# Kernel tuning notes

Hardware: AMD Instinct MI355X
Metric: run time of the kernel (lower is better)

## Reference

```python
import jax, jax.numpy as jnp
import numpy as np

B, S, D, H = 2, 2048, 1024, 16
DH = D // H  # 64, matches Attention's hardcoded d_k=64 scale


def setup_inputs() -> dict:
    key = jax.random.key(0)
    kq, kk, kv, kw, kb = jax.random.split(key, 5)
    return {
        "q": jax.random.normal(kq, (B, S, D), dtype=jnp.float32),
        "k": jax.random.normal(kk, (B, S, D), dtype=jnp.float32),
        "v": jax.random.normal(kv, (B, S, D), dtype=jnp.float32),
        "w_o_w": jax.random.normal(kw, (D, D), dtype=jnp.float32) * 0.02,
        "w_o_b": jax.random.normal(kb, (D,), dtype=jnp.float32) * 0.02,
    }


def _to_heads(x):
    # [B,S,D] -> [B,H,S,DH]
    b, s, d = x.shape
    return x.reshape(b, s, H, DH).transpose(0, 2, 1, 3)


def reference(q, k, v, w_o_w, w_o_b):
    # pre-activation (F.relu) on raw q,k,v
    qh = _to_heads(jax.nn.relu(q))
    kh = _to_heads(jax.nn.relu(k))
    vh = _to_heads(jax.nn.relu(v))
    scale = 1.0 / jnp.sqrt(jnp.asarray(DH, dtype=q.dtype))
    # naive attention: full [B,H,S,S] score matrix, softmax over keys
    scores = jnp.einsum("bhsd,bhtd->bhst", qh, kh) * scale
    probs = jax.nn.softmax(scores, axis=-1)
    attn = jnp.einsum("bhst,bhtd->bhsd", probs, vh)
    # merge heads: [B,H,S,DH] -> [B,S,D]
    out = attn.transpose(0, 2, 1, 3).reshape(B, S, D)
    # output projection (nn.Linear applies x @ W.T + b) then post-activation
    out = out @ w_o_w.T + w_o_b
    return jax.nn.relu(out)
```

## Files before the change

### kernel.cpp

```cpp
#include <hip/hip_runtime.h>
#include <hip/hip_bf16.h>

#define Bc 2
#define Hc 16
#define Sc 2048
#define Dc 1024

typedef __attribute__((ext_vector_type(8))) short s16x8;
typedef __attribute__((ext_vector_type(4))) float f32x4;
typedef __attribute__((ext_vector_type(16))) float f32x16;

#define AS1 __attribute__((address_space(1)))
#define AS3 __attribute__((address_space(3)))

static __device__ __forceinline__ float fexp2(float x) {
#if __has_builtin(__builtin_amdgcn_exp2f)
    return __builtin_amdgcn_exp2f(x);
#else
    float r; asm("v_exp_f32 %0, %1" : "=v"(r) : "v"(x)); return r;
#endif
}

static __device__ __forceinline__ unsigned cvtpk(float lo, float hi) {
    unsigned r; asm("v_cvt_pk_bf16_f32 %0, %1, %2" : "=v"(r) : "v"(lo), "v"(hi));
    return r;
}

static __device__ __forceinline__ void plswap(unsigned &x, unsigned &y) {
#if __has_builtin(__builtin_amdgcn_permlane32_swap)
    typedef __attribute__((ext_vector_type(2))) unsigned int u32x2;
    u32x2 t = __builtin_amdgcn_permlane32_swap(x, y, false, false);
    x = t.x; y = t.y;
#else
    asm volatile("v_permlane32_swap_b32 %0, %1" : "+v"(x), "+v"(y));
#endif
}

static __device__ __forceinline__ unsigned short f2bf(float f) {
    union { float f; unsigned u; } x; x.f = f;
    unsigned r = x.u + 0x7fffu + ((x.u >> 16) & 1u);
    return (unsigned short)(r >> 16);
}

__global__ __launch_bounds__(256) void relu_cvt_heads(const float* __restrict__ src,
                                                      unsigned short* __restrict__ dst,
                                                      float scale) {
    long i = ((long)blockIdx.x * blockDim.x + threadIdx.x) * 4;
    if (i >= (long)Bc * Sc * Dc) return;
    int dh = (int)(i & 63);
    int h  = (int)((i >> 6) & (Hc - 1));
    int s  = (int)((i >> 10) & (Sc - 1));
    int b  = (int)(i >> 21);
    float4 v = *reinterpret_cast<const float4*>(src + i);
    long o = (((long)b * Hc + h) * Sc + s) * 64 + dh;
    ushort4 w;
    w.x = f2bf(fmaxf(v.x, 0.f) * scale);
    w.y = f2bf(fmaxf(v.y, 0.f) * scale);
    w.z = f2bf(fmaxf(v.z, 0.f) * scale);
    w.w = f2bf(fmaxf(v.w, 0.f) * scale);
    *reinterpret_cast<ushort4*>(dst + o) = w;
}

__global__ __launch_bounds__(256) void relu_cvt_vT(const float* __restrict__ v,
                                                   unsigned short* __restrict__ vt) {
    __shared__ unsigned short lds[64][66];
    const int tid = threadIdx.x;
    const int st = blockIdx.x & (Sc / 64 - 1);
    const int bh = blockIdx.x >> 5;
    const int b = bh >> 4, h = bh & 15;
#pragma unroll
    for (int i = 0; i < 4; ++i) {
        int srow = (tid >> 4) + i * 16;
        int scol = (tid & 15) * 4;
        float4 x = *(const float4*)(v + ((long)b * Sc + st * 64 + srow) * Dc + h * 64 + scol);
        lds[srow][scol + 0] = f2bf(fmaxf(x.x, 0.f));
        lds[srow][scol + 1] = f2bf(fmaxf(x.y, 0.f));
        lds[srow][scol + 2] = f2bf(fmaxf(x.z, 0.f));
        lds[srow][scol + 3] = f2bf(fmaxf(x.w, 0.f));
    }
    __syncthreads();
#pragma unroll
    for (int i = 0; i < 2; ++i) {
        int dh = (tid >> 3) + i * 32;
        int sc = (tid & 7) * 8;
        union { unsigned short u[8]; s16x8 v8; } o;
#pragma unroll
        for (int j = 0; j < 8; ++j) o.u[j] = lds[sc + j][dh];
        *(s16x8*)(vt + ((long)bh * 64 + dh) * Sc + st * 64 + sc) = o.v8;
    }
}

__global__ __launch_bounds__(256) void cvt_w(const float* __restrict__ src,
                                             unsigned short* __restrict__ dst) {
    long i = ((long)blockIdx.x * blockDim.x + threadIdx.x) * 4;
    if (i >= (long)Dc * Dc) return;
    float4 v = *reinterpret_cast<const float4*>(src + i);
    ushort4 w;
    w.x = f2bf(v.x); w.y = f2bf(v.y); w.z = f2bf(v.z); w.w = f2bf(v.w);
    *reinterpret_cast<ushort4*>(dst + i) = w;
}

__global__ __launch_bounds__(256, 2) void attn_lds(const unsigned short* __restrict__ qh,
                                                   const unsigned short* __restrict__ kh,
                                                   const unsigned short* __restrict__ vt,
                                                   unsigned short* __restrict__ xout) {
    __shared__ unsigned short Klds[2][64 * 64];
    __shared__ unsigned short Vlds[2][64 * 64];

    const int tid = threadIdx.x;
    const int l = tid & 63, w = tid >> 6;
    const int r32 = l & 31, hl = l >> 5;
    const int job = (blockIdx.x & 7) * 64 + (blockIdx.x >> 3);
    const int qb = job & 15;
    const int bh = job >> 4;

    const unsigned short* Qp = qh + ((long)bh * Sc + qb * 128 + w * 32) * 64;
    const unsigned short* Kp = kh + (long)bh * Sc * 64;
    const unsigned short* Vp = vt + (long)bh * 64 * Sc;

    s16x8 qbf[4];
#pragma unroll
    for (int ds = 0; ds < 4; ++ds)
        qbf[ds] = *(const s16x8*)(Qp + r32 * 64 + ds * 16 + hl * 8);

    f32x16 acc0 = {0,0,0,0,0,0,0,0,0,0,0,0,0,0,0,0};
    f32x16 acc1 = {0,0,0,0,0,0,0,0,0,0,0,0,0,0,0,0};
    float denom = 0.f;

    auto stage = [&](int buf, int kv0) {
#pragma unroll
        for (int j = 0; j < 2; ++j) {
            const int cbase = w * 64 + j * 256;
            const int chunk = cbase + l;
            const int row = chunk >> 3, cc = chunk & 7;
            const int scc = cc ^ (row & 7);
            const unsigned short* ksrc = Kp + (long)(kv0 + row) * 64 + scc * 8;
            const unsigned short* vsrc = Vp + (long)row * Sc + kv0 + scc * 8;
            __builtin_amdgcn_global_load_lds((const AS1 unsigned int*)(const void*)ksrc,
                                             (AS3 unsigned int*)(void*)&Klds[buf][cbase * 8],
                                             16, 0, 0);
            __builtin_amdgcn_global_load_lds((const AS1 unsigned int*)(const void*)vsrc,
                                             (AS3 unsigned int*)(void*)&Vlds[buf][cbase * 8],
                                             16, 0, 0);
        }
    };

    auto compute = [&](int buf) {
        const unsigned short* KB = &Klds[buf][0];
        const unsigned short* VB = &Vlds[buf][0];
        unsigned Bw[4][4];
#pragma unroll
        for (int kt = 0; kt < 2; ++kt) {
            f32x16 st = {0,0,0,0,0,0,0,0,0,0,0,0,0,0,0,0};
#pragma unroll
            for (int ds = 0; ds < 4; ++ds) {
                const int row = kt * 32 + r32;
                const int cc = ((ds * 2 + hl) ^ (row & 7));
                s16x8 ka = *(const s16x8*)(KB + row * 64 + cc * 8);
                st = __builtin_amdgcn_mfma_f32_32x32x16_bf16(ka, qbf[ds], st, 0, 0, 0);
            }
            float p[16];
#pragma unroll
            for (int i = 0; i < 16; ++i) p[i] = fexp2(st[i]);
            denom += (((p[0] + p[1]) + (p[2] + p[3])) + ((p[4] + p[5]) + (p[6] + p[7])))
                   + (((p[8] + p[9]) + (p[10] + p[11])) + ((p[12] + p[13]) + (p[14] + p[15])));
            unsigned a0 = cvtpk(p[0], p[1]),   b0 = cvtpk(p[2], p[3]);
            unsigned c0 = cvtpk(p[4], p[5]),   d0 = cvtpk(p[6], p[7]);
            unsigned a1 = cvtpk(p[8], p[9]),   b1 = cvtpk(p[10], p[11]);
            unsigned c1 = cvtpk(p[12], p[13]), d1 = cvtpk(p[14], p[15]);
            plswap(a0, c0); plswap(b0, d0);
            plswap(a1, c1); plswap(b1, d1);
            Bw[kt * 2 + 0][0] = a0; Bw[kt * 2 + 0][1] = b0;
            Bw[kt * 2 + 0][2] = c0; Bw[kt * 2 + 0][3] = d0;
            Bw[kt * 2 + 1][0] = a1; Bw[kt * 2 + 1][1] = b1;
            Bw[kt * 2 + 1][2] = c1; Bw[kt * 2 + 1][3] = d1;
        }
#pragma unroll
        for (int dt = 0; dt < 2; ++dt) {
#pragma unroll
            for (int s = 0; s < 4; ++s) {
                const int row = dt * 32 + r32;
                const int cc = ((s * 2 + hl) ^ (row & 7));
                s16x8 va = *(const s16x8*)(VB + row * 64 + cc * 8);
                union { unsigned u[4]; s16x8 v8; } bp;
                bp.u[0] = Bw[s][0]; bp.u[1] = Bw[s][1];
                bp.u[2] = Bw[s][2]; bp.u[3] = Bw[s][3];
                if (dt == 0)
                    acc0 = __builtin_amdgcn_mfma_f32_32x32x16_bf16(va, bp.v8, acc0, 0, 0, 0);
                else
                    acc1 = __builtin_amdgcn_mfma_f32_32x32x16_bf16(va, bp.v8, acc1, 0, 0, 0);
            }
        }
    };

    stage(0, 0);
    __syncthreads();
    int cur = 0;
    for (int t = 0; t < Sc / 64 - 1; ++t) {
        stage(cur ^ 1, (t + 1) * 64);
        compute(cur);
        __syncthreads();
        cur ^= 1;
    }
    compute(cur);

    float dn = denom + __shfl_xor(denom, 32);
    const float inv = 1.0f / dn;
    const int b = bh >> 4, h = bh & 15;
    unsigned short* Xrow = xout + ((long)b * Sc + qb * 128 + w * 32 + r32) * Dc + h * 64;
#pragma unroll
    for (int dt = 0; dt < 2; ++dt) {
        const f32x16& A = dt ? acc1 : acc0;
#pragma unroll
        for (int rg = 0; rg < 4; ++rg) {
            unsigned wlo = cvtpk(A[rg * 4 + 0] * inv, A[rg * 4 + 1] * inv);
            unsigned whi = cvtpk(A[rg * 4 + 2] * inv, A[rg * 4 + 3] * inv);
            uint2 wv; wv.x = wlo; wv.y = whi;
            *reinterpret_cast<uint2*>(Xrow + dt * 32 + rg * 8 + hl * 4) = wv;
        }
    }
}

__global__ __launch_bounds__(256, 2) void proj128(const unsigned short* __restrict__ X,
                                                  const unsigned short* __restrict__ Wb,
                                                  const float* __restrict__ bias,
                                                  float* __restrict__ out) {
    __shared__ unsigned short Xlds[2][128 * 64];
    __shared__ unsigned short Wlds[2][64 * 64];

    const int tid = threadIdx.x;
    const int l = tid & 63, w = tid >> 6;
    const int r32 = l & 31, hl = l >> 5;
    const int job = (blockIdx.x & 7) * 64 + (blockIdx.x >> 3);
    const int nb = job & 15;
    const int mb = job >> 4;

    const unsigned short* Xp = X + (long)mb * 128 * Dc;
    const unsigned short* Wp = Wb + (long)nb * 64 * Dc;

    f32x16 acc0 = {0,0,0,0,0,0,0,0,0,0,0,0,0,0,0,0};
    f32x16 acc1 = {0,0,0,0,0,0,0,0,0,0,0,0,0,0,0,0};

    auto stage = [&](int buf, int k0) {
#pragma unroll
        for (int j = 0; j < 4; ++j) {
            const int cbase = w * 256 + j * 64;
            const int chunk = cbase + l;
            const int row = chunk >> 3, cc = chunk & 7;
            const int scc = cc ^ (row & 7);
            const unsigned short* xsrc = Xp + (long)row * Dc + k0 + scc * 8;
            __builtin_amdgcn_global_load_lds((const AS1 unsigned int*)(const void*)xsrc,
                                             (AS3 unsigned int*)(void*)&Xlds[buf][cbase * 8],
                                             16, 0, 0);
        }
#pragma unroll
        for (int j = 0; j < 2; ++j) {
            const int cbase = w * 128 + j * 64;
            const int chunk = cbase + l;
            const int row = chunk >> 3, cc = chunk & 7;
            const int scc = cc ^ (row & 7);
            const unsigned short* wsrc = Wp + (long)row * Dc + k0 + scc * 8;
            __builtin_amdgcn_global_load_lds((const AS1 unsigned int*)(const void*)wsrc,
                                             (AS3 unsigned int*)(void*)&Wlds[buf][cbase * 8],
                                             16, 0, 0);
        }
    };

    auto compute = [&](int buf) {
        const unsigned short* XB = &Xlds[buf][0];
        const unsigned short* WB = &Wlds[buf][0];
#pragma unroll
        for (int ks = 0; ks < 4; ++ks) {
            const int arow = w * 32 + r32;
            const int acc_ = ((ks * 2 + hl) ^ (arow & 7));
            s16x8 af = *(const s16x8*)(XB + arow * 64 + acc_ * 8);
#pragma unroll
            for (int nt = 0; nt < 2; ++nt) {
                const int brow = nt * 32 + r32;
                const int bcc = ((ks * 2 + hl) ^ (brow & 7));
                s16x8 bf = *(const s16x8*)(WB + brow * 64 + bcc * 8);
                if (nt == 0)
                    acc0 = __builtin_amdgcn_mfma_f32_32x32x16_bf16(af, bf, acc0, 0, 0, 0);
                else
                    acc1 = __builtin_amdgcn_mfma_f32_32x32x16_bf16(af, bf, acc1, 0, 0, 0);
            }
        }
    };

    stage(0, 0);
    __syncthreads();
    int cur = 0;
    for (int t = 0; t < Dc / 64 - 1; ++t) {
        stage(cur ^ 1, (t + 1) * 64);
        compute(cur);
        __syncthreads();
        cur ^= 1;
    }
    compute(cur);

#pragma unroll
    for (int nt = 0; nt < 2; ++nt) {
        const f32x16& A = nt ? acc1 : acc0;
        const float bv = bias[nb * 64 + nt * 32 + r32];
#pragma unroll
        for (int j = 0; j < 16; ++j) {
            const int m = (j & 3) + 8 * (j >> 2) + 4 * hl;
            out[((long)(mb * 128 + w * 32 + m)) * Dc + nb * 64 + nt * 32 + r32] =
                fmaxf(A[j] + bv, 0.f);
        }
    }
}

extern "C" void kernel_launch(void* const* d_in, const int* in_sizes, int n_in,
                              void* d_out, int out_size, void* d_ws, size_t ws_size,
                              hipStream_t stream) {
    const float* q    = (const float*)d_in[0];
    const float* k    = (const float*)d_in[1];
    const float* v    = (const float*)d_in[2];
    const float* w    = (const float*)d_in[3];
    const float* bias = (const float*)d_in[4];
    float* out = (float*)d_out;

    unsigned short* ws = (unsigned short*)d_ws;
    unsigned short* qh = ws;
    unsigned short* kh = qh + 4194304;
    unsigned short* vt = kh + 4194304;
    unsigned short* wb = vt + 4194304;
    unsigned short* X  = wb + 1048576;

    const float QSCALE = 0.125f * 1.44269504088896340736f;
    relu_cvt_heads<<<4096, 256, 0, stream>>>(q, qh, QSCALE);
    relu_cvt_heads<<<4096, 256, 0, stream>>>(k, kh, 1.0f);
    relu_cvt_vT<<<1024, 256, 0, stream>>>(v, vt);
    cvt_w<<<1024, 256, 0, stream>>>(w, wb);
    attn_lds<<<Bc * Hc * (Sc / 128), 256, 0, stream>>>(qh, kh, vt, X);
    proj128<<<(Bc * Sc / 128) * (Dc / 64), 256, 0, stream>>>(X, wb, bias, out);
}
```

Baseline: 83.21 us.

## Triple-buffer LDS staging with vmcnt waits and MFMA priority hints

Both the attention and projection kernels move from double-buffered to triple-buffered LDS staging. Each iteration waits only for the oldest tile's loads (s_waitcnt vmcnt) and then hits a single barrier, which keeps two tiles of global loads in flight and drops the second __syncthreads per iteration. The last two iterations issue wrap-around dummy loads so the loop body stays uniform. The MFMA sections are also wrapped in s_setprio to favour matrix issue. LDS use per block rises by half, which may reduce occupancy (notably proj128 at 72KB), and the extra tail loads add a little traffic.

```diff
diff --git a/kernel.cpp b/kernel.cpp
--- a/kernel.cpp
+++ b/kernel.cpp
@@ -12,6 +12,8 @@
 
 #define AS1 __attribute__((address_space(1)))
 #define AS3 __attribute__((address_space(3)))
+
+#define WAITVMC(N) asm volatile("s_waitcnt vmcnt(" #N ")" ::: "memory")
 
 static __device__ __forceinline__ float fexp2(float x) {
 #if __has_builtin(__builtin_amdgcn_exp2f)
@@ -104,8 +106,8 @@
                                                    const unsigned short* __restrict__ kh,
                                                    const unsigned short* __restrict__ vt,
                                                    unsigned short* __restrict__ xout) {
-    __shared__ unsigned short Klds[2][64 * 64];
-    __shared__ unsigned short Vlds[2][64 * 64];
+    __shared__ unsigned short Klds[3][64 * 64];
+    __shared__ unsigned short Vlds[3][64 * 64];
 
     const int tid = threadIdx.x;
     const int l = tid & 63, w = tid >> 6;
@@ -152,6 +154,7 @@
 #pragma unroll
         for (int kt = 0; kt < 2; ++kt) {
             f32x16 st = {0,0,0,0,0,0,0,0,0,0,0,0,0,0,0,0};
+            __builtin_amdgcn_s_setprio(1);
 #pragma unroll
             for (int ds = 0; ds < 4; ++ds) {
                 const int row = kt * 32 + r32;
@@ -159,6 +162,7 @@
                 s16x8 ka = *(const s16x8*)(KB + row * 64 + cc * 8);
                 st = __builtin_amdgcn_mfma_f32_32x32x16_bf16(ka, qbf[ds], st, 0, 0, 0);
             }
+            __builtin_amdgcn_s_setprio(0);
             float p[16];
 #pragma unroll
             for (int i = 0; i < 16; ++i) p[i] = fexp2(st[i]);
@@ -175,6 +179,7 @@
             Bw[kt * 2 + 1][0] = a1; Bw[kt * 2 + 1][1] = b1;
             Bw[kt * 2 + 1][2] = c1; Bw[kt * 2 + 1][3] = d1;
         }
+        __builtin_amdgcn_s_setprio(1);
 #pragma unroll
         for (int dt = 0; dt < 2; ++dt) {
 #pragma unroll
@@ -191,18 +196,21 @@
                     acc1 = __builtin_amdgcn_mfma_f32_32x32x16_bf16(va, bp.v8, acc1, 0, 0, 0);
             }
         }
+        __builtin_amdgcn_s_setprio(0);
     };
 
     stage(0, 0);
-    __syncthreads();
-    int cur = 0;
-    for (int t = 0; t < Sc / 64 - 1; ++t) {
-        stage(cur ^ 1, (t + 1) * 64);
-        compute(cur);
-        __syncthreads();
-        cur ^= 1;
-    }
-    compute(cur);
+    stage(1, 64);
+    int bcur = 0;
+    for (int t = 0; t < Sc / 64; ++t) {
+        WAITVMC(4);
+        __builtin_amdgcn_s_barrier();
+        __builtin_amdgcn_sched_barrier(0);
+        int bn = bcur + 2; if (bn >= 3) bn -= 3;
+        stage(bn, ((t + 2) & (Sc / 64 - 1)) * 64);
+        compute(bcur);
+        if (++bcur == 3) bcur = 0;
+    }
 
     float dn = denom + __shfl_xor(denom, 32);
     const float inv = 1.0f / dn;
@@ -225,8 +233,8 @@
                                                   const unsigned short* __restrict__ Wb,
                                                   const float* __restrict__ bias,
                                                   float* __restrict__ out) {
-    __shared__ unsigned short Xlds[2][128 * 64];
-    __shared__ unsigned short Wlds[2][64 * 64];
+    __shared__ unsigned short Xlds[3][128 * 64];
+    __shared__ unsigned short Wlds[3][64 * 64];
 
     const int tid = threadIdx.x;
     const int l = tid & 63, w = tid >> 6;
@@ -288,15 +296,17 @@
     };
 
     stage(0, 0);
-    __syncthreads();
-    int cur = 0;
-    for (int t = 0; t < Dc / 64 - 1; ++t) {
-        stage(cur ^ 1, (t + 1) * 64);
-        compute(cur);
-        __syncthreads();
-        cur ^= 1;
-    }
-    compute(cur);
+    stage(1, 64);
+    int bcur = 0;
+    for (int t = 0; t < Dc / 64; ++t) {
+        WAITVMC(6);
+        __builtin_amdgcn_s_barrier();
+        __builtin_amdgcn_sched_barrier(0);
+        int bn = bcur + 2; if (bn >= 3) bn -= 3;
+        stage(bn, ((t + 2) & (Dc / 64 - 1)) * 64);
+        compute(bcur);
+        if (++bcur == 3) bcur = 0;
+    }
 
 #pragma unroll
     for (int nt = 0; nt < 2; ++nt) {
```

Result: no change. 84.21 us (+1.2%).

## Double KV tile to 128 and software-pipeline QK, softmax, PV sub-tiles

Applied to the files above, without the earlier changes.

Each iteration now stages a 128-key tile of K and V into LDS instead of 64, which halves the number of barriers and stage calls. Compute is split into four 32-key sub-tiles, interleaved so that the QK MFMAs of the next sub-tile, the exp/convert of the current one and the PV MFMAs of an earlier one overlap. s_setprio is raised around the MFMA sections. The cost is double the LDS per block (64KB), which may limit occupancy, plus higher register pressure from the extra live score tiles.

```diff
diff --git a/kernel.cpp b/kernel.cpp
--- a/kernel.cpp
+++ b/kernel.cpp
@@ -104,8 +104,8 @@
                                                    const unsigned short* __restrict__ kh,
                                                    const unsigned short* __restrict__ vt,
                                                    unsigned short* __restrict__ xout) {
-    __shared__ unsigned short Klds[2][64 * 64];
-    __shared__ unsigned short Vlds[2][64 * 64];
+    __shared__ unsigned short Klds[2][128 * 64];
+    __shared__ unsigned short Vlds[2][64 * 128];
 
     const int tid = threadIdx.x;
     const int l = tid & 63, w = tid >> 6;
@@ -129,75 +129,102 @@
 
     auto stage = [&](int buf, int kv0) {
 #pragma unroll
-        for (int j = 0; j < 2; ++j) {
-            const int cbase = w * 64 + j * 256;
+        for (int j = 0; j < 4; ++j) {
+            const int cbase = w * 256 + j * 64;
             const int chunk = cbase + l;
-            const int row = chunk >> 3, cc = chunk & 7;
-            const int scc = cc ^ (row & 7);
-            const unsigned short* ksrc = Kp + (long)(kv0 + row) * 64 + scc * 8;
-            const unsigned short* vsrc = Vp + (long)row * Sc + kv0 + scc * 8;
-            __builtin_amdgcn_global_load_lds((const AS1 unsigned int*)(const void*)ksrc,
-                                             (AS3 unsigned int*)(void*)&Klds[buf][cbase * 8],
-                                             16, 0, 0);
-            __builtin_amdgcn_global_load_lds((const AS1 unsigned int*)(const void*)vsrc,
-                                             (AS3 unsigned int*)(void*)&Vlds[buf][cbase * 8],
-                                             16, 0, 0);
-        }
-    };
-
-    auto compute = [&](int buf) {
-        const unsigned short* KB = &Klds[buf][0];
-        const unsigned short* VB = &Vlds[buf][0];
-        unsigned Bw[4][4];
-#pragma unroll
-        for (int kt = 0; kt < 2; ++kt) {
-            f32x16 st = {0,0,0,0,0,0,0,0,0,0,0,0,0,0,0,0};
-#pragma unroll
-            for (int ds = 0; ds < 4; ++ds) {
-                const int row = kt * 32 + r32;
-                const int cc = ((ds * 2 + hl) ^ (row & 7));
-                s16x8 ka = *(const s16x8*)(KB + row * 64 + cc * 8);
-                st = __builtin_amdgcn_mfma_f32_32x32x16_bf16(ka, qbf[ds], st, 0, 0, 0);
+            {
+                const int row = chunk >> 3, cc = chunk & 7;
+                const int scc = cc ^ (row & 7);
+                const unsigned short* ksrc = Kp + (long)(kv0 + row) * 64 + scc * 8;
+                __builtin_amdgcn_global_load_lds((const AS1 unsigned int*)(const void*)ksrc,
+                                                 (AS3 unsigned int*)(void*)&Klds[buf][cbase * 8],
+                                                 16, 0, 0);
             }
-            float p[16];
-#pragma unroll
-            for (int i = 0; i < 16; ++i) p[i] = fexp2(st[i]);
-            denom += (((p[0] + p[1]) + (p[2] + p[3])) + ((p[4] + p[5]) + (p[6] + p[7])))
-                   + (((p[8] + p[9]) + (p[10] + p[11])) + ((p[12] + p[13]) + (p[14] + p[15])));
-            unsigned a0 = cvtpk(p[0], p[1]),   b0 = cvtpk(p[2], p[3]);
-            unsigned c0 = cvtpk(p[4], p[5]),   d0 = cvtpk(p[6], p[7]);
-            unsigned a1 = cvtpk(p[8], p[9]),   b1 = cvtpk(p[10], p[11]);
-            unsigned c1 = cvtpk(p[12], p[13]), d1 = cvtpk(p[14], p[15]);
-            plswap(a0, c0); plswap(b0, d0);
-            plswap(a1, c1); plswap(b1, d1);
-            Bw[kt * 2 + 0][0] = a0; Bw[kt * 2 + 0][1] = b0;
-            Bw[kt * 2 + 0][2] = c0; Bw[kt * 2 + 0][3] = d0;
-            Bw[kt * 2 + 1][0] = a1; Bw[kt * 2 + 1][1] = b1;
-            Bw[kt * 2 + 1][2] = c1; Bw[kt * 2 + 1][3] = d1;
-        }
-#pragma unroll
-        for (int dt = 0; dt < 2; ++dt) {
-#pragma unroll
-            for (int s = 0; s < 4; ++s) {
+            {
+                const int row = chunk >> 4, cc = chunk & 15;
+                const int scc = cc ^ (row & 7);
+                const unsigned short* vsrc = Vp + (long)row * Sc + kv0 + scc * 8;
+                __builtin_amdgcn_global_load_lds((const AS1 unsigned int*)(const void*)vsrc,
+                                                 (AS3 unsigned int*)(void*)&Vlds[buf][cbase * 8],
+                                                 16, 0, 0);
+            }
+        }
+    };
+
+    auto qkSub = [&](const unsigned short* KB, int sub) {
+        f32x16 st = {0,0,0,0,0,0,0,0,0,0,0,0,0,0,0,0};
+        __builtin_amdgcn_s_setprio(1);
+#pragma unroll
+        for (int ds = 0; ds < 4; ++ds) {
+            const int row = sub * 32 + r32;
+            const int cc = ((ds * 2 + hl) ^ (row & 7));
+            s16x8 ka = *(const s16x8*)(KB + row * 64 + cc * 8);
+            st = __builtin_amdgcn_mfma_f32_32x32x16_bf16(ka, qbf[ds], st, 0, 0, 0);
+        }
+        __builtin_amdgcn_s_setprio(0);
+        return st;
+    };
+
+    auto smSub = [&](const f32x16& st, unsigned* Bw) {
+        float p[16];
+#pragma unroll
+        for (int i = 0; i < 16; ++i) p[i] = fexp2(st[i]);
+        denom += (((p[0] + p[1]) + (p[2] + p[3])) + ((p[4] + p[5]) + (p[6] + p[7])))
+               + (((p[8] + p[9]) + (p[10] + p[11])) + ((p[12] + p[13]) + (p[14] + p[15])));
+        unsigned a0 = cvtpk(p[0], p[1]),   b0 = cvtpk(p[2], p[3]);
+        unsigned c0 = cvtpk(p[4], p[5]),   d0 = cvtpk(p[6], p[7]);
+        unsigned a1 = cvtpk(p[8], p[9]),   b1 = cvtpk(p[10], p[11]);
+        unsigned c1 = cvtpk(p[12], p[13]), d1 = cvtpk(p[14], p[15]);
+        plswap(a0, c0); plswap(b0, d0);
+        plswap(a1, c1); plswap(b1, d1);
+        Bw[0] = a0; Bw[1] = b0; Bw[2] = c0; Bw[3] = d0;
+        Bw[4] = a1; Bw[5] = b1; Bw[6] = c1; Bw[7] = d1;
+    };
+
+    auto pvSub = [&](const unsigned short* VB, int sub, const unsigned* Bw) {
+        __builtin_amdgcn_s_setprio(1);
+#pragma unroll
+        for (int ks = 0; ks < 2; ++ks) {
+            union { unsigned u[4]; s16x8 v8; } bp;
+            bp.u[0] = Bw[ks * 4 + 0]; bp.u[1] = Bw[ks * 4 + 1];
+            bp.u[2] = Bw[ks * 4 + 2]; bp.u[3] = Bw[ks * 4 + 3];
+#pragma unroll
+            for (int dt = 0; dt < 2; ++dt) {
                 const int row = dt * 32 + r32;
-                const int cc = ((s * 2 + hl) ^ (row & 7));
-                s16x8 va = *(const s16x8*)(VB + row * 64 + cc * 8);
-                union { unsigned u[4]; s16x8 v8; } bp;
-                bp.u[0] = Bw[s][0]; bp.u[1] = Bw[s][1];
-                bp.u[2] = Bw[s][2]; bp.u[3] = Bw[s][3];
+                const int cc = ((sub * 4 + ks * 2 + hl) ^ (row & 7));
+                s16x8 va = *(const s16x8*)(VB + row * 128 + cc * 8);
                 if (dt == 0)
                     acc0 = __builtin_amdgcn_mfma_f32_32x32x16_bf16(va, bp.v8, acc0, 0, 0, 0);
                 else
                     acc1 = __builtin_amdgcn_mfma_f32_32x32x16_bf16(va, bp.v8, acc1, 0, 0, 0);
             }
         }
+        __builtin_amdgcn_s_setprio(0);
+    };
+
+    auto compute = [&](int buf) {
+        const unsigned short* KB = &Klds[buf][0];
+        const unsigned short* VB = &Vlds[buf][0];
+        unsigned B0[8], B1[8], B2[8], B3[8];
+        f32x16 s0 = qkSub(KB, 0);
+        f32x16 s1 = qkSub(KB, 1);
+        smSub(s0, B0);
+        f32x16 s2 = qkSub(KB, 2);
+        smSub(s1, B1);
+        pvSub(VB, 0, B0);
+        f32x16 s3 = qkSub(KB, 3);
+        smSub(s2, B2);
+        pvSub(VB, 1, B1);
+        smSub(s3, B3);
+        pvSub(VB, 2, B2);
+        pvSub(VB, 3, B3);
     };
 
     stage(0, 0);
     __syncthreads();
     int cur = 0;
-    for (int t = 0; t < Sc / 64 - 1; ++t) {
-        stage(cur ^ 1, (t + 1) * 64);
+    for (int t = 0; t < Sc / 128 - 1; ++t) {
+        stage(cur ^ 1, (t + 1) * 128);
         compute(cur);
         __syncthreads();
         cur ^= 1;
```

New measurement: 82.31 us. No clear change (-1.1%).

## Give each attention wave 64 query rows to reuse K/V LDS fragments

Applied to the files above, without the earlier changes.

The attention kernel now runs 2 waves per block (128 threads), and each wave handles 64 query rows as two 32-row subtiles instead of 32 rows. Each K and V fragment read from LDS then feeds two MFMAs, which halves LDS read traffic per unit of compute. Priority hints (s_setprio) are placed around the MFMA sections to help overlap them with the exp/convert work of other waves. The costs are doubled accumulator register pressure and only half as many waves per block to hide latency.

```diff
diff --git a/kernel.cpp b/kernel.cpp
--- a/kernel.cpp
+++ b/kernel.cpp
@@ -100,7 +100,7 @@
     *reinterpret_cast<ushort4*>(dst + i) = w;
 }
 
-__global__ __launch_bounds__(256, 2) void attn_lds(const unsigned short* __restrict__ qh,
+__global__ __launch_bounds__(128, 1) void attn_q64(const unsigned short* __restrict__ qh,
                                                    const unsigned short* __restrict__ kh,
                                                    const unsigned short* __restrict__ vt,
                                                    unsigned short* __restrict__ xout) {
@@ -114,82 +114,104 @@
     const int qb = job & 15;
     const int bh = job >> 4;
 
-    const unsigned short* Qp = qh + ((long)bh * Sc + qb * 128 + w * 32) * 64;
+    const unsigned short* Qp = qh + ((long)bh * Sc + qb * 128 + w * 64) * 64;
     const unsigned short* Kp = kh + (long)bh * Sc * 64;
     const unsigned short* Vp = vt + (long)bh * 64 * Sc;
 
-    s16x8 qbf[4];
-#pragma unroll
-    for (int ds = 0; ds < 4; ++ds)
-        qbf[ds] = *(const s16x8*)(Qp + r32 * 64 + ds * 16 + hl * 8);
-
-    f32x16 acc0 = {0,0,0,0,0,0,0,0,0,0,0,0,0,0,0,0};
-    f32x16 acc1 = {0,0,0,0,0,0,0,0,0,0,0,0,0,0,0,0};
-    float denom = 0.f;
+    s16x8 qbf[2][4];
+#pragma unroll
+    for (int qi = 0; qi < 2; ++qi)
+#pragma unroll
+        for (int ds = 0; ds < 4; ++ds)
+            qbf[qi][ds] = *(const s16x8*)(Qp + (qi * 32 + r32) * 64 + ds * 16 + hl * 8);
+
+    f32x16 acc00 = {0,0,0,0,0,0,0,0,0,0,0,0,0,0,0,0};
+    f32x16 acc01 = {0,0,0,0,0,0,0,0,0,0,0,0,0,0,0,0};
+    f32x16 acc10 = {0,0,0,0,0,0,0,0,0,0,0,0,0,0,0,0};
+    f32x16 acc11 = {0,0,0,0,0,0,0,0,0,0,0,0,0,0,0,0};
+    float denom0 = 0.f, denom1 = 0.f;
 
     auto stage = [&](int buf, int kv0) {
 #pragma unroll
-        for (int j = 0; j < 2; ++j) {
-            const int cbase = w * 64 + j * 256;
-            const int chunk = cbase + l;
+        for (int j = 0; j < 4; ++j) {
+            const int chunk = j * 128 + tid;
             const int row = chunk >> 3, cc = chunk & 7;
             const int scc = cc ^ (row & 7);
             const unsigned short* ksrc = Kp + (long)(kv0 + row) * 64 + scc * 8;
             const unsigned short* vsrc = Vp + (long)row * Sc + kv0 + scc * 8;
             __builtin_amdgcn_global_load_lds((const AS1 unsigned int*)(const void*)ksrc,
-                                             (AS3 unsigned int*)(void*)&Klds[buf][cbase * 8],
+                                             (AS3 unsigned int*)(void*)&Klds[buf][chunk * 8],
                                              16, 0, 0);
             __builtin_amdgcn_global_load_lds((const AS1 unsigned int*)(const void*)vsrc,
-                                             (AS3 unsigned int*)(void*)&Vlds[buf][cbase * 8],
+                                             (AS3 unsigned int*)(void*)&Vlds[buf][chunk * 8],
                                              16, 0, 0);
         }
+    };
+
+    auto smSub = [&](const f32x16& st, unsigned* Bw, float& dn) {
+        float p[16];
+#pragma unroll
+        for (int i = 0; i < 16; ++i) p[i] = fexp2(st[i]);
+        dn += (((p[0] + p[1]) + (p[2] + p[3])) + ((p[4] + p[5]) + (p[6] + p[7])))
+            + (((p[8] + p[9]) + (p[10] + p[11])) + ((p[12] + p[13]) + (p[14] + p[15])));
+        unsigned a0 = cvtpk(p[0], p[1]),   b0 = cvtpk(p[2], p[3]);
+        unsigned c0 = cvtpk(p[4], p[5]),   d0 = cvtpk(p[6], p[7]);
+        unsigned a1 = cvtpk(p[8], p[9]),   b1 = cvtpk(p[10], p[11]);
+        unsigned c1 = cvtpk(p[12], p[13]), d1 = cvtpk(p[14], p[15]);
+        plswap(a0, c0); plswap(b0, d0);
+        plswap(a1, c1); plswap(b1, d1);
+        Bw[0] = a0; Bw[1] = b0; Bw[2] = c0; Bw[3] = d0;
+        Bw[4] = a1; Bw[5] = b1; Bw[6] = c1; Bw[7] = d1;
     };
 
     auto compute = [&](int buf) {
         const unsigned short* KB = &Klds[buf][0];
         const unsigned short* VB = &Vlds[buf][0];
-        unsigned Bw[4][4];
 #pragma unroll
         for (int kt = 0; kt < 2; ++kt) {
-            f32x16 st = {0,0,0,0,0,0,0,0,0,0,0,0,0,0,0,0};
+            s16x8 ka[4];
 #pragma unroll
             for (int ds = 0; ds < 4; ++ds) {
                 const int row = kt * 32 + r32;
                 const int cc = ((ds * 2 + hl) ^ (row & 7));
-                s16x8 ka = *(const s16x8*)(KB + row * 64 + cc * 8);
-                st = __builtin_amdgcn_mfma_f32_32x32x16_bf16(ka, qbf[ds], st, 0, 0, 0);
+                ka[ds] = *(const s16x8*)(KB + row * 64 + cc * 8);
             }
-            float p[16];
-#pragma unroll
-            for (int i = 0; i < 16; ++i) p[i] = fexp2(st[i]);
-            denom += (((p[0] + p[1]) + (p[2] + p[3])) + ((p[4] + p[5]) + (p[6] + p[7])))
-                   + (((p[8] + p[9]) + (p[10] + p[11])) + ((p[12] + p[13]) + (p[14] + p[15])));
-            unsigned a0 = cvtpk(p[0], p[1]),   b0 = cvtpk(p[2], p[3]);
-            unsigned c0 = cvtpk(p[4], p[5]),   d0 = cvtpk(p[6], p[7]);
-            unsigned a1 = cvtpk(p[8], p[9]),   b1 = cvtpk(p[10], p[11]);
-            unsigned c1 = cvtpk(p[12], p[13]), d1 = cvtpk(p[14], p[15]);
-            plswap(a0, c0); plswap(b0, d0);
-            plswap(a1, c1); plswap(b1, d1);
-            Bw[kt * 2 + 0][0] = a0; Bw[kt * 2 + 0][1] = b0;
-            Bw[kt * 2 + 0][2] = c0; Bw[kt * 2 + 0][3] = d0;
-            Bw[kt * 2 + 1][0] = a1; Bw[kt * 2 + 1][1] = b1;
-            Bw[kt * 2 + 1][2] = c1; Bw[kt * 2 + 1][3] = d1;
-        }
-#pragma unroll
-        for (int dt = 0; dt < 2; ++dt) {
-#pragma unroll
-            for (int s = 0; s < 4; ++s) {
-                const int row = dt * 32 + r32;
-                const int cc = ((s * 2 + hl) ^ (row & 7));
-                s16x8 va = *(const s16x8*)(VB + row * 64 + cc * 8);
-                union { unsigned u[4]; s16x8 v8; } bp;
-                bp.u[0] = Bw[s][0]; bp.u[1] = Bw[s][1];
-                bp.u[2] = Bw[s][2]; bp.u[3] = Bw[s][3];
-                if (dt == 0)
-                    acc0 = __builtin_amdgcn_mfma_f32_32x32x16_bf16(va, bp.v8, acc0, 0, 0, 0);
-                else
-                    acc1 = __builtin_amdgcn_mfma_f32_32x32x16_bf16(va, bp.v8, acc1, 0, 0, 0);
+            f32x16 st0 = {0,0,0,0,0,0,0,0,0,0,0,0,0,0,0,0};
+            f32x16 st1 = {0,0,0,0,0,0,0,0,0,0,0,0,0,0,0,0};
+            __builtin_amdgcn_s_setprio(1);
+#pragma unroll
+            for (int ds = 0; ds < 4; ++ds)
+                st0 = __builtin_amdgcn_mfma_f32_32x32x16_bf16(ka[ds], qbf[0][ds], st0, 0, 0, 0);
+#pragma unroll
+            for (int ds = 0; ds < 4; ++ds)
+                st1 = __builtin_amdgcn_mfma_f32_32x32x16_bf16(ka[ds], qbf[1][ds], st1, 0, 0, 0);
+            __builtin_amdgcn_s_setprio(0);
+            unsigned Bw0[8], Bw1[8];
+            smSub(st0, Bw0, denom0);
+            smSub(st1, Bw1, denom1);
+            __builtin_amdgcn_s_setprio(1);
+#pragma unroll
+            for (int ks = 0; ks < 2; ++ks) {
+                union { unsigned u[4]; s16x8 v8; } bp0, bp1;
+                bp0.u[0] = Bw0[ks * 4 + 0]; bp0.u[1] = Bw0[ks * 4 + 1];
+                bp0.u[2] = Bw0[ks * 4 + 2]; bp0.u[3] = Bw0[ks * 4 + 3];
+                bp1.u[0] = Bw1[ks * 4 + 0]; bp1.u[1] = Bw1[ks * 4 + 1];
+                bp1.u[2] = Bw1[ks * 4 + 2]; bp1.u[3] = Bw1[ks * 4 + 3];
+#pragma unroll
+                for (int dt = 0; dt < 2; ++dt) {
+                    const int row = dt * 32 + r32;
+                    const int cc = ((kt * 4 + ks * 2 + hl) ^ (row & 7));
+                    s16x8 va = *(const s16x8*)(VB + row * 64 + cc * 8);
+                    if (dt == 0) {
+                        acc00 = __builtin_amdgcn_mfma_f32_32x32x16_bf16(va, bp0.v8, acc00, 0, 0, 0);
+                        acc10 = __builtin_amdgcn_mfma_f32_32x32x16_bf16(va, bp1.v8, acc10, 0, 0, 0);
+                    } else {
+                        acc01 = __builtin_amdgcn_mfma_f32_32x32x16_bf16(va, bp0.v8, acc01, 0, 0, 0);
+                        acc11 = __builtin_amdgcn_mfma_f32_32x32x16_bf16(va, bp1.v8, acc11, 0, 0, 0);
+                    }
+                }
             }
+            __builtin_amdgcn_s_setprio(0);
         }
     };
 
@@ -204,19 +226,24 @@
     }
     compute(cur);
 
-    float dn = denom + __shfl_xor(denom, 32);
-    const float inv = 1.0f / dn;
     const int b = bh >> 4, h = bh & 15;
-    unsigned short* Xrow = xout + ((long)b * Sc + qb * 128 + w * 32 + r32) * Dc + h * 64;
-#pragma unroll
-    for (int dt = 0; dt < 2; ++dt) {
-        const f32x16& A = dt ? acc1 : acc0;
-#pragma unroll
-        for (int rg = 0; rg < 4; ++rg) {
-            unsigned wlo = cvtpk(A[rg * 4 + 0] * inv, A[rg * 4 + 1] * inv);
-            unsigned whi = cvtpk(A[rg * 4 + 2] * inv, A[rg * 4 + 3] * inv);
-            uint2 wv; wv.x = wlo; wv.y = whi;
-            *reinterpret_cast<uint2*>(Xrow + dt * 32 + rg * 8 + hl * 4) = wv;
+#pragma unroll
+    for (int qi = 0; qi < 2; ++qi) {
+        float dref = qi ? denom1 : denom0;
+        float dn = dref + __shfl_xor(dref, 32);
+        const float inv = 1.0f / dn;
+        unsigned short* Xrow = xout +
+            ((long)b * Sc + qb * 128 + w * 64 + qi * 32 + r32) * Dc + h * 64;
+#pragma unroll
+        for (int dt = 0; dt < 2; ++dt) {
+            const f32x16& A = qi ? (dt ? acc11 : acc10) : (dt ? acc01 : acc00);
+#pragma unroll
+            for (int rg = 0; rg < 4; ++rg) {
+                unsigned wlo = cvtpk(A[rg * 4 + 0] * inv, A[rg * 4 + 1] * inv);
+                unsigned whi = cvtpk(A[rg * 4 + 2] * inv, A[rg * 4 + 3] * inv);
+                uint2 wv; wv.x = wlo; wv.y = whi;
+                *reinterpret_cast<uint2*>(Xrow + dt * 32 + rg * 8 + hl * 4) = wv;
+            }
         }
     }
 }
@@ -333,6 +360,6 @@
     relu_cvt_heads<<<4096, 256, 0, stream>>>(k, kh, 1.0f);
     relu_cvt_vT<<<1024, 256, 0, stream>>>(v, vt);
     cvt_w<<<1024, 256, 0, stream>>>(w, wb);
-    attn_lds<<<Bc * Hc * (Sc / 128), 256, 0, stream>>>(qh, kh, vt, X);
+    attn_q64<<<Bc * Hc * (Sc / 128), 128, 0, stream>>>(qh, kh, vt, X);
     proj128<<<(Bc * Sc / 128) * (Dc / 64), 256, 0, stream>>>(X, wb, bias, out);
 }
```

Measured after the change: 121.5 us. +46.1%, slower.
